# Performance work log

Hardware: AMD Instinct MI355X
Metric: run time of the kernel (lower is better)

Reference implementation:

```python
import jax, jax.numpy as jnp
import numpy as np

HIDDEN = 2048
NUM_EXPERTS = 8
TOP_K = 2
CAPACITY_FACTOR = 1.5
B, S = 2, 2048


def setup_inputs() -> dict:
    key = jax.random.key(0)
    k0, k1, k2 = jax.random.split(key, 3)
    hidden_states = jax.random.normal(k0, (B, S, HIDDEN), dtype=jnp.float32)
    # xavier-normal init per nn.init.xavier_normal_
    std1 = float(np.sqrt(2.0 / (HIDDEN + HIDDEN)))
    std2 = float(np.sqrt(2.0 / (HIDDEN + NUM_EXPERTS)))
    w1 = jax.random.normal(k1, (HIDDEN, HIDDEN), dtype=jnp.float32) * std1
    b1 = jnp.zeros((HIDDEN,), dtype=jnp.float32)
    w2 = jax.random.normal(k2, (NUM_EXPERTS, HIDDEN), dtype=jnp.float32) * std2
    b2 = jnp.zeros((NUM_EXPERTS,), dtype=jnp.float32)
    return {"hidden_states": hidden_states, "w1": w1, "b1": b1, "w2": w2, "b2": b2}


def reference(hidden_states, w1, b1, w2, b2):
    Bs, Ss, H = hidden_states.shape
    E, K = NUM_EXPERTS, TOP_K
    T = Bs * Ss
    capacity = int(T * CAPACITY_FACTOR * K / E)

    # router MLP: Linear -> ReLU -> Linear (dropout=0 -> identity)
    h = jax.nn.relu(jnp.einsum('bsh,oh->bso', hidden_states, w1) + b1)
    router_logits = jnp.einsum('bsh,eh->bse', h, w2) + b2  # [B,S,E]
    router_probs = jax.nn.softmax(router_logits, axis=-1)

    top_k_probs, top_k_indices = jax.lax.top_k(router_probs, K)  # [B,S,K]
    top_k_probs = top_k_probs / (jnp.sum(top_k_probs, axis=-1, keepdims=True) + 1e-8)

    # dispatch/combine: tokens claim capacity slots in (b,s,k) order.
    fe = top_k_indices.reshape(-1)            # [T*K] expert id per assignment
    fp = top_k_probs.reshape(-1)              # [T*K] prob per assignment
    onehot = (fe[:, None] == jnp.arange(E)[None, :]).astype(jnp.int32)  # [T*K,E]
    cum = jnp.cumsum(onehot, axis=0)          # running per-expert counts
    pos = jnp.take_along_axis(cum, fe[:, None], axis=1)[:, 0] - 1        # slot index
    valid = pos < capacity
    pos_c = jnp.minimum(pos, capacity - 1)
    tok = jnp.arange(T * K) // K              # flat token index

    dispatch = jnp.zeros((T, E, capacity), dtype=router_probs.dtype)
    combine = jnp.zeros((T, E, capacity), dtype=router_probs.dtype)
    dispatch = dispatch.at[tok, fe, pos_c].add(valid.astype(router_probs.dtype))
    combine = combine.at[tok, fe, pos_c].add(jnp.where(valid, fp, 0.0))
    dispatch_tensor = dispatch.reshape(Bs, Ss, E, capacity)
    combine_tensor = combine.reshape(Bs, Ss, E, capacity)

    # load-balancing aux loss
    router_prob_per_expert = jnp.mean(router_probs, axis=(0, 1))          # [E]
    expert_mask = jax.nn.one_hot(top_k_indices, E, dtype=router_probs.dtype)  # [B,S,K,E]
    expert_usage_rate = jnp.mean(expert_mask, axis=(0, 1, 2))             # [E]
    aux_loss = jnp.sum(router_prob_per_expert * expert_usage_rate) * E

    return dispatch_tensor, combine_tensor, router_probs, aux_loss
```

## Files before the change

kernel.cpp:

```cpp
#include <hip/hip_runtime.h>

#define HID   2048
#define NE    8
#define NK    2
#define NTOK  4096
#define NASS  (NTOK * NK)
#define CAP   1536
#define DISP_ELEMS ((size_t)NTOK * NE * CAP)
#define KBLK  (HID / 32)
#define NXBLK (NTOK * KBLK)
#define ZCHUNKS_PER_BLK 49152

typedef __bf16 bf16x8 __attribute__((ext_vector_type(8)));
typedef float  f32x4  __attribute__((ext_vector_type(4)));

typedef const __attribute__((address_space(1))) unsigned int GUint;
typedef       __attribute__((address_space(3))) unsigned int LUint;

__device__ __forceinline__ void gload16(const void* g, void* l) {
    __builtin_amdgcn_global_load_lds((GUint*)g, (LUint*)l, 16, 0, 0);
}

__global__ __launch_bounds__(256) void split_kernel(
    const float* __restrict__ X, const float* __restrict__ W1,
    __bf16* __restrict__ Xs, __bf16* __restrict__ Ws)
{
    int g = blockIdx.x * 256 + threadIdx.x;
    int blk = g >> 2, sub = g & 3;
    const float* s;
    __bf16* d;
    if (blk < NXBLK) { s = X  + (size_t)blk * 32 + sub * 8;
                       d = Xs + (size_t)blk * 64; }
    else             { s = W1 + (size_t)(blk - NXBLK) * 32 + sub * 8;
                       d = Ws + (size_t)(blk - NXBLK) * 64; }
    float x[8];
    float4 v0 = ((const float4*)s)[0], v1 = ((const float4*)s)[1];
    x[0]=v0.x; x[1]=v0.y; x[2]=v0.z; x[3]=v0.w;
    x[4]=v1.x; x[5]=v1.y; x[6]=v1.z; x[7]=v1.w;
    bf16x8 h8, l8;
#pragma unroll
    for (int j = 0; j < 8; ++j) {
        __bf16 h = (__bf16)x[j];
        h8[j] = h;
        l8[j] = (__bf16)(x[j] - (float)h);
    }
    *(bf16x8*)(d + sub * 8)      = h8;
    *(bf16x8*)(d + 32 + sub * 8) = l8;
}

__global__ __launch_bounds__(256, 3) void gemm1_mfma_kernel(
    const __bf16* __restrict__ Xs,
    const __bf16* __restrict__ Ws,
    const float* __restrict__ b1, float* __restrict__ hout,
    float* __restrict__ zout)
{
    __shared__ __bf16 As[128 * 64];
    __shared__ __bf16 Bs[128 * 64];

    const int tid  = threadIdx.x;
    const int wid  = tid >> 6;
    const int lane = tid & 63;

    int wg  = blockIdx.x;
    int swz = (wg & 7) * 64 + (wg >> 3);
    const int bx = swz & 15;
    const int by = swz >> 4;
    const int brow = by * 128;
    const int bcol = bx * 128;

    const int srow   = lane >> 3;
    const int sslot  = lane & 7;

    const int wr = wid >> 1, wc = wid & 1;
    const int fr = lane & 15;
    const int fc = lane >> 4;

    f32x4* zdst = (f32x4*)zout + (size_t)blockIdx.x * ZCHUNKS_PER_BLK + tid;
    const f32x4 zz = (f32x4)0.f;

    f32x4 acc[4][4];
#pragma unroll
    for (int m = 0; m < 4; ++m)
#pragma unroll
        for (int n = 0; n < 4; ++n) acc[m][n] = (f32x4)0.f;

    for (int b = 0; b < KBLK; ++b) {
#pragma unroll
        for (int i = 0; i < 4; ++i) {
            int ra = wid * 32 + i * 8 + srow;
            int ca = sslot ^ (ra & 7);
            gload16(Xs + ((size_t)(brow + ra) * KBLK + b) * 64 + ca * 8,
                    &As[(wid * 32 + i * 8) * 64]);
            int cb = sslot ^ (ra & 7);
            gload16(Ws + ((size_t)(bcol + ra) * KBLK + b) * 64 + cb * 8,
                    &Bs[(wid * 32 + i * 8) * 64]);
        }
        __syncthreads();

        {
            f32x4* z = zdst + (size_t)b * 768;
            __builtin_nontemporal_store(zz, z);
            __builtin_nontemporal_store(zz, z + 256);
            __builtin_nontemporal_store(zz, z + 512);
        }

        bf16x8 bh[4], bl[4];
#pragma unroll
        for (int n = 0; n < 4; ++n) {
            int rb = wc * 64 + n * 16 + fr;
            bh[n] = *(const bf16x8*)&Bs[rb * 64 + ((fc       ^ (rb & 7)) << 3)];
            bl[n] = *(const bf16x8*)&Bs[rb * 64 + (((4 + fc) ^ (rb & 7)) << 3)];
        }
#pragma unroll
        for (int m = 0; m < 4; ++m) {
            int ra = wr * 64 + m * 16 + fr;
            bf16x8 ah = *(const bf16x8*)&As[ra * 64 + ((fc       ^ (ra & 7)) << 3)];
            bf16x8 al = *(const bf16x8*)&As[ra * 64 + (((4 + fc) ^ (ra & 7)) << 3)];
#pragma unroll
            for (int n = 0; n < 4; ++n) {
                f32x4 c = acc[m][n];
                c = __builtin_amdgcn_mfma_f32_16x16x32_bf16(ah, bh[n], c, 0, 0, 0);
                c = __builtin_amdgcn_mfma_f32_16x16x32_bf16(al, bh[n], c, 0, 0, 0);
                c = __builtin_amdgcn_mfma_f32_16x16x32_bf16(ah, bl[n], c, 0, 0, 0);
                acc[m][n] = c;
            }
        }
        __syncthreads();
    }

#pragma unroll
    for (int m = 0; m < 4; ++m) {
#pragma unroll
        for (int n = 0; n < 4; ++n) {
            int row = brow + wr * 64 + m * 16 + fc * 4;
            int col = bcol + wc * 64 + n * 16 + fr;
            float bias = b1[col];
#pragma unroll
            for (int j = 0; j < 4; ++j) {
                float v = acc[m][n][j] + bias;
                hout[(size_t)(row + j) * HID + col] = fmaxf(v, 0.f);
            }
        }
    }
}

__global__ __launch_bounds__(256) void router_kernel(
    const float* __restrict__ hbuf, const float* __restrict__ w2,
    const float* __restrict__ b2, float* __restrict__ probs_out,
    int* __restrict__ topk_e, float* __restrict__ topk_p)
{
    const int t    = (blockIdx.x * 256 + threadIdx.x) >> 6;
    const int lane = threadIdx.x & 63;
    const float* hrow = hbuf + (size_t)t * HID;

    float acc[NE];
#pragma unroll
    for (int e = 0; e < NE; ++e) acc[e] = 0.f;

#pragma unroll
    for (int j = 0; j < HID / (64 * 4); ++j) {
        const int o = (j * 64 + lane) * 4;
        float4 hv = *(const float4*)(hrow + o);
#pragma unroll
        for (int e = 0; e < NE; ++e) {
            float4 wv = *(const float4*)(w2 + e * HID + o);
            acc[e] += hv.x * wv.x + hv.y * wv.y + hv.z * wv.z + hv.w * wv.w;
        }
    }
#pragma unroll
    for (int m = 32; m > 0; m >>= 1)
#pragma unroll
        for (int e = 0; e < NE; ++e) acc[e] += __shfl_xor(acc[e], m);

    if (lane == 0) {
        float lg[NE];
        float mx = -1e30f;
#pragma unroll
        for (int e = 0; e < NE; ++e) { lg[e] = acc[e] + b2[e]; mx = fmaxf(mx, lg[e]); }
        float sum = 0.f;
#pragma unroll
        for (int e = 0; e < NE; ++e) { lg[e] = expf(lg[e] - mx); sum += lg[e]; }
        float inv = 1.f / sum;
        float p[NE];
#pragma unroll
        for (int e = 0; e < NE; ++e) { p[e] = lg[e] * inv; probs_out[t * NE + e] = p[e]; }
        int e1 = 0;
#pragma unroll
        for (int e = 1; e < NE; ++e) if (p[e] > p[e1]) e1 = e;
        int e2 = -1;
#pragma unroll
        for (int e = 0; e < NE; ++e) if (e != e1 && (e2 < 0 || p[e] > p[e2])) e2 = e;
        float denom = p[e1] + p[e2] + 1e-8f;
        topk_e[t * NK + 0] = e1;
        topk_e[t * NK + 1] = e2;
        topk_p[t * NK + 0] = p[e1] / denom;
        topk_p[t * NK + 1] = p[e2] / denom;
    }
}

__global__ __launch_bounds__(256) void finalize_kernel(
    const int* __restrict__ topk_e, const float* __restrict__ topk_p,
    const float* __restrict__ probs, float* __restrict__ dispatch,
    float* __restrict__ combine, float* __restrict__ aux_out)
{
    const int tid = threadIdx.x;
    __shared__ int   sc[256][NE];
    __shared__ float tot[NE];
    __shared__ float rps[256][NE];

    int cnt[NE];
#pragma unroll
    for (int e = 0; e < NE; ++e) cnt[e] = 0;
    const int base = tid * 32;
    int eloc[32];
    for (int i = 0; i < 32; ++i) { eloc[i] = topk_e[base + i]; cnt[eloc[i]]++; }
#pragma unroll
    for (int e = 0; e < NE; ++e) sc[tid][e] = cnt[e];
    __syncthreads();
    if (tid < NE) {
        int run = 0;
        for (int i = 0; i < 256; ++i) { int v = sc[i][tid]; sc[i][tid] = run; run += v; }
        tot[tid] = (float)run;
    }
    __syncthreads();
    int run[NE];
#pragma unroll
    for (int e = 0; e < NE; ++e) run[e] = sc[tid][e];
    for (int i = 0; i < 32; ++i) {
        const int a = base + i;
        const int e = eloc[i];
        const int p = run[e]++;
        if (p < CAP) {
            const int t = a >> 1;
            const size_t off = ((size_t)t * NE + e) * CAP + p;
            dispatch[off] = 1.0f;
            combine[off]  = topk_p[a];
        }
    }

    float ps[NE];
#pragma unroll
    for (int e = 0; e < NE; ++e) ps[e] = 0.f;
    for (int t = tid; t < NTOK; t += 256)
#pragma unroll
        for (int e = 0; e < NE; ++e) ps[e] += probs[t * NE + e];
#pragma unroll
    for (int e = 0; e < NE; ++e) rps[tid][e] = ps[e];
    __syncthreads();
    for (int s = 128; s > 0; s >>= 1) {
        if (tid < s) {
#pragma unroll
            for (int e = 0; e < NE; ++e) rps[tid][e] += rps[tid + s][e];
        }
        __syncthreads();
    }
    if (tid == 0) {
        float aux = 0.f;
#pragma unroll
        for (int e = 0; e < NE; ++e)
            aux += (rps[0][e] / (float)NTOK) * (tot[e] / (float)NASS);
        aux_out[0] = aux * (float)NE;
    }
}

extern "C" void kernel_launch(void* const* d_in, const int* in_sizes, int n_in,
                              void* d_out, int out_size, void* d_ws, size_t ws_size,
                              hipStream_t stream)
{
    const float* X  = (const float*)d_in[0];
    const float* w1 = (const float*)d_in[1];
    const float* b1 = (const float*)d_in[2];
    const float* w2 = (const float*)d_in[3];
    const float* b2 = (const float*)d_in[4];

    float* out      = (float*)d_out;
    float* dispatch = out;
    float* combine  = out + DISP_ELEMS;
    float* probs    = out + 2 * DISP_ELEMS;
    float* aux      = out + 2 * DISP_ELEMS + (size_t)NTOK * NE;

    __bf16* Xs     = (__bf16*)d_ws;
    __bf16* Ws     = Xs + (size_t)NTOK * HID * 2;
    float*  hbuf   = (float*)(Ws + (size_t)HID * HID * 2);
    int*    topk_e = (int*)(hbuf + (size_t)NTOK * HID);
    float*  topk_p = (float*)(topk_e + NASS);

    split_kernel<<<((NTOK + HID) * KBLK * 4) / 256, 256, 0, stream>>>(X, w1, Xs, Ws);
    gemm1_mfma_kernel<<<512, 256, 0, stream>>>(Xs, Ws, b1, hbuf, out);
    router_kernel<<<NTOK / 4, 256, 0, stream>>>(hbuf, w2, b2, probs, topk_e, topk_p);
    finalize_kernel<<<1, 256, 0, stream>>>(topk_e, topk_p, probs, dispatch, combine, aux);
}
```

Baseline: 509.3 us.

## Fuse second router projection into GEMM1 epilogue with per-panel partial logits

The ReLU output of the first GEMM is no longer written to a 32 MB hidden buffer. Instead, each GEMM block multiplies its tile by the matching w2 columns, reduces across lanes and in shared memory, and writes per-column-panel partial logits. A small new kernel sums the 16 panels, adds b2, and does softmax and top-k. This removes the full write and re-read of h, at the cost of extra epilogue shuffles, shared memory and registers in the GEMM, and a summation order that differs from the reference.

```diff
diff --git a/kernel.cpp b/kernel.cpp
--- a/kernel.cpp
+++ b/kernel.cpp
@@ -9,6 +9,7 @@
 #define DISP_ELEMS ((size_t)NTOK * NE * CAP)
 #define KBLK  (HID / 32)
 #define NXBLK (NTOK * KBLK)
+#define NPANEL 16
 #define ZCHUNKS_PER_BLK 49152
 
 typedef __bf16 bf16x8 __attribute__((ext_vector_type(8)));
@@ -51,11 +52,14 @@
 __global__ __launch_bounds__(256, 3) void gemm1_mfma_kernel(
     const __bf16* __restrict__ Xs,
     const __bf16* __restrict__ Ws,
-    const float* __restrict__ b1, float* __restrict__ hout,
+    const float* __restrict__ b1,
+    const float* __restrict__ w2,
+    float* __restrict__ partial,
     float* __restrict__ zout)
 {
     __shared__ __bf16 As[128 * 64];
     __shared__ __bf16 Bs[128 * 64];
+    __shared__ float  Part[2][64][2][NE];
 
     const int tid  = threadIdx.x;
     const int wid  = tid >> 6;
@@ -91,8 +95,7 @@
             int ca = sslot ^ (ra & 7);
             gload16(Xs + ((size_t)(brow + ra) * KBLK + b) * 64 + ca * 8,
                     &As[(wid * 32 + i * 8) * 64]);
-            int cb = sslot ^ (ra & 7);
-            gload16(Ws + ((size_t)(bcol + ra) * KBLK + b) * 64 + cb * 8,
+            gload16(Ws + ((size_t)(bcol + ra) * KBLK + b) * 64 + ca * 8,
                     &Bs[(wid * 32 + i * 8) * 64]);
         }
         __syncthreads();
@@ -128,74 +131,85 @@
         __syncthreads();
     }
 
+    float w2v[NE][4], bias4[4];
+#pragma unroll
+    for (int n = 0; n < 4; ++n) {
+        int col = bcol + wc * 64 + n * 16 + fr;
+        bias4[n] = b1[col];
+#pragma unroll
+        for (int e = 0; e < NE; ++e) w2v[e][n] = w2[e * HID + col];
+    }
 #pragma unroll
     for (int m = 0; m < 4; ++m) {
 #pragma unroll
-        for (int n = 0; n < 4; ++n) {
-            int row = brow + wr * 64 + m * 16 + fc * 4;
-            int col = bcol + wc * 64 + n * 16 + fr;
-            float bias = b1[col];
-#pragma unroll
-            for (int j = 0; j < 4; ++j) {
-                float v = acc[m][n][j] + bias;
-                hout[(size_t)(row + j) * HID + col] = fmaxf(v, 0.f);
+        for (int j = 0; j < 4; ++j) {
+            float esum[NE];
+#pragma unroll
+            for (int e = 0; e < NE; ++e) esum[e] = 0.f;
+#pragma unroll
+            for (int n = 0; n < 4; ++n) {
+                float h = fmaxf(acc[m][n][j] + bias4[n], 0.f);
+#pragma unroll
+                for (int e = 0; e < NE; ++e) esum[e] += h * w2v[e][n];
             }
-        }
-    }
-}
-
-__global__ __launch_bounds__(256) void router_kernel(
-    const float* __restrict__ hbuf, const float* __restrict__ w2,
-    const float* __restrict__ b2, float* __restrict__ probs_out,
-    int* __restrict__ topk_e, float* __restrict__ topk_p)
-{
-    const int t    = (blockIdx.x * 256 + threadIdx.x) >> 6;
-    const int lane = threadIdx.x & 63;
-    const float* hrow = hbuf + (size_t)t * HID;
-
-    float acc[NE];
-#pragma unroll
-    for (int e = 0; e < NE; ++e) acc[e] = 0.f;
-
-#pragma unroll
-    for (int j = 0; j < HID / (64 * 4); ++j) {
-        const int o = (j * 64 + lane) * 4;
-        float4 hv = *(const float4*)(hrow + o);
-#pragma unroll
-        for (int e = 0; e < NE; ++e) {
-            float4 wv = *(const float4*)(w2 + e * HID + o);
-            acc[e] += hv.x * wv.x + hv.y * wv.y + hv.z * wv.z + hv.w * wv.w;
-        }
-    }
-#pragma unroll
-    for (int m = 32; m > 0; m >>= 1)
-#pragma unroll
-        for (int e = 0; e < NE; ++e) acc[e] += __shfl_xor(acc[e], m);
-
-    if (lane == 0) {
-        float lg[NE];
-        float mx = -1e30f;
-#pragma unroll
-        for (int e = 0; e < NE; ++e) { lg[e] = acc[e] + b2[e]; mx = fmaxf(mx, lg[e]); }
-        float sum = 0.f;
-#pragma unroll
-        for (int e = 0; e < NE; ++e) { lg[e] = expf(lg[e] - mx); sum += lg[e]; }
-        float inv = 1.f / sum;
-        float p[NE];
-#pragma unroll
-        for (int e = 0; e < NE; ++e) { p[e] = lg[e] * inv; probs_out[t * NE + e] = p[e]; }
-        int e1 = 0;
-#pragma unroll
-        for (int e = 1; e < NE; ++e) if (p[e] > p[e1]) e1 = e;
-        int e2 = -1;
-#pragma unroll
-        for (int e = 0; e < NE; ++e) if (e != e1 && (e2 < 0 || p[e] > p[e2])) e2 = e;
-        float denom = p[e1] + p[e2] + 1e-8f;
-        topk_e[t * NK + 0] = e1;
-        topk_e[t * NK + 1] = e2;
-        topk_p[t * NK + 0] = p[e1] / denom;
-        topk_p[t * NK + 1] = p[e2] / denom;
-    }
+#pragma unroll
+            for (int msk = 1; msk < 16; msk <<= 1)
+#pragma unroll
+                for (int e = 0; e < NE; ++e) esum[e] += __shfl_xor(esum[e], msk);
+            if (fr == 0) {
+                int row64 = m * 16 + fc * 4 + j;
+#pragma unroll
+                for (int e = 0; e < NE; ++e) Part[wr][row64][wc][e] = esum[e];
+            }
+        }
+    }
+    __syncthreads();
+#pragma unroll
+    for (int it = 0; it < 4; ++it) {
+        int idx = it * 256 + tid;
+        int row128 = idx >> 3, e = idx & 7;
+        float v = Part[row128 >> 6][row128 & 63][0][e]
+                + Part[row128 >> 6][row128 & 63][1][e];
+        partial[((size_t)bx * NTOK + brow + row128) * NE + e] = v;
+    }
+}
+
+__global__ __launch_bounds__(256) void logits_topk_kernel(
+    const float* __restrict__ partial, const float* __restrict__ b2,
+    float* __restrict__ probs_out, int* __restrict__ topk_e,
+    float* __restrict__ topk_p)
+{
+    const int t = blockIdx.x * 256 + threadIdx.x;
+    float lg[NE];
+#pragma unroll
+    for (int e = 0; e < NE; ++e) lg[e] = b2[e];
+    for (int p = 0; p < NPANEL; ++p) {
+        const float4* src = (const float4*)(partial + ((size_t)p * NTOK + t) * NE);
+        float4 a = src[0], b = src[1];
+        lg[0] += a.x; lg[1] += a.y; lg[2] += a.z; lg[3] += a.w;
+        lg[4] += b.x; lg[5] += b.y; lg[6] += b.z; lg[7] += b.w;
+    }
+    float mx = -1e30f;
+#pragma unroll
+    for (int e = 0; e < NE; ++e) mx = fmaxf(mx, lg[e]);
+    float sum = 0.f;
+#pragma unroll
+    for (int e = 0; e < NE; ++e) { lg[e] = expf(lg[e] - mx); sum += lg[e]; }
+    float inv = 1.f / sum;
+    float p[NE];
+#pragma unroll
+    for (int e = 0; e < NE; ++e) { p[e] = lg[e] * inv; probs_out[t * NE + e] = p[e]; }
+    int e1 = 0;
+#pragma unroll
+    for (int e = 1; e < NE; ++e) if (p[e] > p[e1]) e1 = e;
+    int e2 = -1;
+#pragma unroll
+    for (int e = 0; e < NE; ++e) if (e != e1 && (e2 < 0 || p[e] > p[e2])) e2 = e;
+    float denom = p[e1] + p[e2] + 1e-8f;
+    topk_e[t * NK + 0] = e1;
+    topk_e[t * NK + 1] = e2;
+    topk_p[t * NK + 0] = p[e1] / denom;
+    topk_p[t * NK + 1] = p[e2] / denom;
 }
 
 __global__ __launch_bounds__(256) void finalize_kernel(
@@ -279,14 +293,14 @@
     float* probs    = out + 2 * DISP_ELEMS;
     float* aux      = out + 2 * DISP_ELEMS + (size_t)NTOK * NE;
 
-    __bf16* Xs     = (__bf16*)d_ws;
-    __bf16* Ws     = Xs + (size_t)NTOK * HID * 2;
-    float*  hbuf   = (float*)(Ws + (size_t)HID * HID * 2);
-    int*    topk_e = (int*)(hbuf + (size_t)NTOK * HID);
-    float*  topk_p = (float*)(topk_e + NASS);
+    __bf16* Xs      = (__bf16*)d_ws;
+    __bf16* Ws      = Xs + (size_t)NTOK * HID * 2;
+    float*  partial = (float*)(Ws + (size_t)HID * HID * 2);
+    int*    topk_e  = (int*)(partial + (size_t)NPANEL * NTOK * NE);
+    float*  topk_p  = (float*)(topk_e + NASS);
 
     split_kernel<<<((NTOK + HID) * KBLK * 4) / 256, 256, 0, stream>>>(X, w1, Xs, Ws);
-    gemm1_mfma_kernel<<<512, 256, 0, stream>>>(Xs, Ws, b1, hbuf, out);
-    router_kernel<<<NTOK / 4, 256, 0, stream>>>(hbuf, w2, b2, probs, topk_e, topk_p);
+    gemm1_mfma_kernel<<<512, 256, 0, stream>>>(Xs, Ws, b1, w2, partial, out);
+    logits_topk_kernel<<<NTOK / 256, 256, 0, stream>>>(partial, b2, probs, topk_e, topk_p);
     finalize_kernel<<<1, 256, 0, stream>>>(topk_e, topk_p, probs, dispatch, combine, aux);
 }
```

Result: no change. 501.2 us (-1.6%).
